# Kernel tuning notes

Hardware: AMD Instinct MI355X
Metric: run time of the kernel (lower is better)

The kernel has to match this reference:

```python
import jax, jax.numpy as jnp
import numpy as np

H = 56; W = 56; WS = 7; SHIFT = 3; C = 128; NH = 4; HD = C // NH
N = WS * WS; NW = (H // WS) * (W // WS); B = 64; HID = 4 * C
ALPHA = (1, 2, 4, 8); SCALE = HD ** -0.5


def _rel_index_np():
    coords = np.stack(np.meshgrid(np.arange(WS), np.arange(WS), indexing="ij"))
    cf = coords.reshape(2, -1)
    rel = (cf[:, :, None] - cf[:, None, :]).transpose(1, 2, 0).copy()
    rel[:, :, 0] += WS - 1
    rel[:, :, 1] += WS - 1
    rel[:, :, 0] *= 2 * WS - 1
    return rel.sum(-1).astype(np.int32)  # (N, N)


def _attn_mask_np():
    img = np.zeros((1, H, W, 1), np.float32)
    cnt = 0
    sl = (slice(0, -WS), slice(-WS, -SHIFT), slice(-SHIFT, None))
    for hs in sl:
        for ws in sl:
            img[:, hs, ws, :] = cnt
            cnt += 1
    mw = img.reshape(1, H // WS, WS, W // WS, WS, 1).transpose(0, 1, 3, 2, 4, 5).reshape(-1, N)
    am = mw[:, None, :] - mw[:, :, None]
    return np.where(am != 0, -100.0, 0.0).astype(np.float32)  # (NW, N, N)


def setup_inputs() -> dict:
    key = jax.random.key(0)
    ks = jax.random.split(key, 8)
    p = lambda k, shp, s=0.02: jax.random.normal(k, shp, jnp.float32) * s
    return {
        "x": jax.random.normal(ks[0], (B, H * W, C), jnp.float32),
        "gumbel_weights": jax.nn.softmax(jax.random.normal(ks[1], (4,), jnp.float32)),
        "norm1_w": jnp.ones((C,), jnp.float32), "norm1_b": jnp.zeros((C,), jnp.float32),
        "qkv_w": p(ks[2], (3 * C, C)), "qkv_b": jnp.zeros((3 * C,), jnp.float32),
        "rel_bias_table": p(ks[3], ((2 * WS - 1) ** 2, NH)),
        "proj_w": p(ks[4], (C, C)), "proj_b": jnp.zeros((C,), jnp.float32),
        "attn_mask": jnp.asarray(_attn_mask_np()),
        "norm2_w": jnp.ones((C,), jnp.float32), "norm2_b": jnp.zeros((C,), jnp.float32),
        "fc1_w": p(ks[5], (HID, C)), "fc1_b": jnp.zeros((HID,), jnp.float32),
        "fc2_w": p(ks[6], (C, HID)), "fc2_b": jnp.zeros((C,), jnp.float32),
        "rel_index": jnp.asarray(_rel_index_np()),
    }


def _ln(x, w, b, eps=1e-5):
    mu = x.mean(-1, keepdims=True)
    var = ((x - mu) ** 2).mean(-1, keepdims=True)
    return (x - mu) * jax.lax.rsqrt(var + eps) * w + b


def _win_part(x):  # (B,H,W,C) -> (B*NW, N, C)
    b = x.shape[0]
    x = x.reshape(b, H // WS, WS, W // WS, WS, C).transpose(0, 1, 3, 2, 4, 5)
    return x.reshape(-1, N, C)


def _win_rev(w, b):  # (b*NW, N, C) -> (b,H,W,C)
    x = w.reshape(b, H // WS, W // WS, WS, WS, C).transpose(0, 1, 3, 2, 4, 5)
    return x.reshape(b, H, W, C)


def _window_attn(xw, qkv_w, qkv_b, bias, mask, proj_w, proj_b):
    b = xw.shape[0]
    qkv = (xw @ qkv_w.T + qkv_b).reshape(b, N, 3, NH, HD).transpose(2, 0, 3, 1, 4)
    q, k, v = qkv[0] * SCALE, qkv[1], qkv[2]  # (b,NH,N,HD)
    a = jnp.einsum("bhnd,bhmd->bhnm", q, k) + bias[None]
    a = (a.reshape(b // NW, NW, NH, N, N) + mask[None, :, None]).reshape(b, NH, N, N)
    a = jax.nn.softmax(a, axis=-1)
    o = jnp.einsum("bhnm,bhmd->bhnd", a, v).transpose(0, 2, 1, 3).reshape(b, N, C)
    return o @ proj_w.T + proj_b


def _forward(x, gw, n1w, n1b, qkv_w, qkv_b, rbt, pw, pb, am, n2w, n2b, f1w, f1b, f2w, f2b, rel_index):
    shortcut = x
    xs = _ln(x, n1w, n1b).reshape(B, H, W, C)
    xs = jnp.roll(xs, (-SHIFT, -SHIFT), axis=(1, 2))  # cyclic shift
    xw = _win_part(xs)  # (B*NW, N, C)
    bias = rbt[rel_index.reshape(-1)].reshape(N, N, NH).transpose(2, 0, 1)  # (NH,N,N)
    half = xw.shape[0] // 2
    xw_l, xw_s = xw[:half], xw[half:]
    # large half: full-width window attention
    y_l = _window_attn(xw_l, qkv_w, qkv_b, bias, am, pw, pb)
    # small half: gumbel-gated slimmable branches (zero channels beyond C//alpha in/out)
    ch = jnp.arange(C)
    y_s = jnp.zeros_like(xw_s)
    for i, a in enumerate(ALPHA):
        if a > NH:
            continue
        cm = (ch < C // a).astype(xw.dtype)
        yb = _window_attn(xw_s * cm, qkv_w, qkv_b, bias, am, pw, pb) * cm
        y_s = y_s + yb * gw[i]
    attn_out = jnp.concatenate([y_l, y_s], axis=0)
    xr = _win_rev(attn_out, B)
    xr = jnp.roll(xr, (SHIFT, SHIFT), axis=(1, 2)).reshape(B, H * W, C)
    x = shortcut + xr
    # MLP with gumbel-gated slimmable small half (matches Mlp.forward)
    xn = _ln(x, n2w, n2b)
    xn_l, xn_s = xn[: B // 2], xn[B // 2 :]
    m_l = jax.nn.gelu(xn_l @ f1w.T + f1b, approximate=False) @ f2w.T + f2b
    m_s = jnp.zeros_like(xn_s)
    for i, a in enumerate(ALPHA):
        if a > NH:
            continue
        cm = (ch < C // a).astype(xn.dtype)
        yb = (jax.nn.gelu((xn_s * cm) @ f1w.T + f1b, approximate=False) @ f2w.T + f2b) * cm
        m_s = m_s + yb * gw[i]
    mlp_out = jnp.concatenate([m_l, m_s], axis=0)
    return x + mlp_out


def reference(x, gumbel_weights, norm1_w, norm1_b, qkv_w, qkv_b, rel_bias_table, proj_w, proj_b, attn_mask, norm2_w, norm2_b, fc1_w, fc1_b, fc2_w, fc2_b, rel_index):
    return _forward(x, gumbel_weights, norm1_w, norm1_b, qkv_w, qkv_b, rel_bias_table, proj_w, proj_b, attn_mask, norm2_w, norm2_b, fc1_w, fc1_b, fc2_w, fc2_b, rel_index)
```

## Files before the change

kernel.cpp:

```cpp
#include <hip/hip_runtime.h>
#include <hip/hip_bf16.h>

#define SHIFT_ 3
#define SCALE_ 0.17677669529663687f
#define NTOK   200704
#define NWIN   4096

typedef short v8s __attribute__((ext_vector_type(8)));
typedef float v4f __attribute__((ext_vector_type(4)));
#define MFMA16(a, b, c) __builtin_amdgcn_mfma_f32_16x16x32_bf16(a, b, c, 0, 0, 0)

static __device__ __forceinline__ unsigned short f2bf(float f) {
    union { float f; unsigned int u; } v; v.f = f;
    unsigned int u = v.u;
    unsigned int r = u + 0x7FFFu + ((u >> 16) & 1u);
    return (unsigned short)(r >> 16);
}
static __device__ __forceinline__ float wsum(float v) {
    #pragma unroll
    for (int o = 32; o; o >>= 1) v += __shfl_xor(v, o);
    return v;
}
static __device__ __forceinline__ float gelu_f(float v) {
    float w = v * v;
    float t = v * fmaf(w, 0.07135481283f, 1.595769122f);
    float e = __expf(-t);
    return v * __builtin_amdgcn_rcpf(1.f + e);
}

#define WS_COMB  67108864
#define WS_WQKV  71303168
#define WS_WPROJ 71401472
#define WS_F1W   71434240
#define WS_F2W   71565312

__global__ __launch_bounds__(256) void k_prep(
    const float* __restrict__ amask, const float* __restrict__ rbt,
    const int* __restrict__ relidx,
    const float* __restrict__ qkvw, const float* __restrict__ projw,
    const float* __restrict__ f1w, const float* __restrict__ f2w,
    float* __restrict__ comb, unsigned short* __restrict__ wqkv,
    unsigned short* __restrict__ wproj, unsigned short* __restrict__ f1wb,
    unsigned short* __restrict__ f2wb, unsigned short* __restrict__ xw) {
    int idx = blockIdx.x * 256 + threadIdx.x;
    if (idx < 1048576) {
        int wpos = idx >> 14;
        int h = (idx >> 12) & 3;
        int i = (idx >> 6) & 63;
        int j = idx & 63;
        float v;
        if (j >= 49) v = -1e30f;
        else if (i >= 49) v = 0.f;
        else v = amask[wpos * 2401 + i * 49 + j] + rbt[relidx[i * 49 + j] * 4 + h];
        comb[idx] = v;
    } else if (idx < 1048576 + 49152) {
        int k = idx - 1048576; wqkv[k] = f2bf(qkvw[k]);
    } else if (idx < 1048576 + 49152 + 16384) {
        int k = idx - (1048576 + 49152); wproj[k] = f2bf(projw[k]);
    } else if (idx < 1048576 + 49152 + 16384 + 65536) {
        int k = idx - (1048576 + 49152 + 16384); f1wb[k] = f2bf(f1w[k]);
    } else if (idx < 1048576 + 49152 + 16384 + 65536 + 65536) {
        int k = idx - (1048576 + 49152 + 16384 + 65536); f2wb[k] = f2bf(f2w[k]);
    } else {
        int k = idx - 1245184;
        if (k < 983040) {
            int win = k / 240, r = k - win * 240;
            uint4 z = make_uint4(0u, 0u, 0u, 0u);
            *(uint4*)((char*)xw + (size_t)win * 16384 + 12544 + (size_t)r * 16) = z;
        }
    }
}

__global__ __launch_bounds__(256) void k_ln1(const float* __restrict__ x,
                                             const float* __restrict__ nw,
                                             const float* __restrict__ nb,
                                             unsigned short* __restrict__ xw) {
    int tok  = blockIdx.x * 4 + (threadIdx.x >> 6);
    int lane = threadIdx.x & 63;
    int win = tok / 49, t = tok - win * 49;
    int bb = win >> 6, wh = (win >> 3) & 7, ww = win & 7;
    int i = t / 7, j = t - i * 7;
    int h  = wh * 7 + i + SHIFT_; if (h  >= 56) h  -= 56;
    int w2 = ww * 7 + j + SHIFT_; if (w2 >= 56) w2 -= 56;
    const float* src = x + ((size_t)bb * 3136 + h * 56 + w2) * 128;
    float v0 = src[lane], v1 = src[lane + 64];
    float mu = wsum(v0 + v1) * (1.f / 128.f);
    float d0 = v0 - mu, d1 = v1 - mu;
    float var = wsum(d0 * d0 + d1 * d1) * (1.f / 128.f);
    float inv = rsqrtf(var + 1e-5f);
    unsigned short* dst = xw + (size_t)win * 8192 + t * 128;
    dst[lane]      = f2bf(d0 * inv * nw[lane]      + nb[lane]);
    dst[lane + 64] = f2bf(d1 * inv * nw[lane + 64] + nb[lane + 64]);
}

__global__ __launch_bounds__(256) void k_ln2(const float* __restrict__ x2,
                                             const float* __restrict__ nw,
                                             const float* __restrict__ nb,
                                             unsigned short* __restrict__ xn) {
    int tok  = blockIdx.x * 4 + (threadIdx.x >> 6);
    int lane = threadIdx.x & 63;
    const float* src = x2 + (size_t)tok * 128;
    float v0 = src[lane], v1 = src[lane + 64];
    float mu = wsum(v0 + v1) * (1.f / 128.f);
    float d0 = v0 - mu, d1 = v1 - mu;
    float var = wsum(d0 * d0 + d1 * d1) * (1.f / 128.f);
    float inv = rsqrtf(var + 1e-5f);
    unsigned short* dst = xn + (size_t)tok * 128;
    dst[lane]      = f2bf(d0 * inv * nw[lane]      + nb[lane]);
    dst[lane + 64] = f2bf(d1 * inv * nw[lane + 64] + nb[lane + 64]);
}

template<int KA>
__device__ __forceinline__ void attn_pass(
    const v8s (&ax)[4][4],
    const unsigned short* __restrict__ wqkv, const float* __restrict__ qkvb,
    const float* __restrict__ comb,
    const unsigned short* __restrict__ wproj, const float* __restrict__ pbias,
    float wgt, int wpos, int wv, int li, int lg,
    unsigned short* __restrict__ s_q, unsigned short* __restrict__ s_k,
    unsigned short* __restrict__ s_v, unsigned short* __restrict__ pw_,
    v4f (&yacc)[2][4])
{
    const v4f z4 = {0.f, 0.f, 0.f, 0.f};
    constexpr int Ca = KA * 32;

    #pragma unroll 2
    for (int nt = 0; nt < 6; nt++) {
        const int ntg = wv * 6 + nt, o0 = ntg * 16;
        v4f acc[4] = {z4, z4, z4, z4};
        #pragma unroll
        for (int k = 0; k < KA; k++) {
            v8s b = *(const v8s*)(wqkv + (o0 + li) * 128 + k * 32 + lg * 8);
            #pragma unroll
            for (int m = 0; m < 4; m++) acc[m] = MFMA16(ax[m][k], b, acc[m]);
        }
        float bo = qkvb[o0 + li];
        if (ntg < 16) {
            unsigned short* dst = (ntg < 8) ? s_q : s_k;
            const int oc = (ntg < 8) ? o0 : o0 - 128;
            const float scl = (ntg < 8) ? SCALE_ : 1.f;
            #pragma unroll
            for (int m = 0; m < 4; m++)
                #pragma unroll
                for (int r = 0; r < 4; r++)
                    dst[(m * 16 + lg * 4 + r) * 136 + oc + li] =
                        f2bf((acc[m][r] + bo) * scl);
        } else {
            const int d = (ntg - 16) * 16 + li;
            #pragma unroll
            for (int m = 0; m < 4; m++) {
                int t0_ = m * 16 + lg * 4;
                unsigned int p0 = (unsigned int)f2bf(acc[m][0] + bo) |
                                  ((unsigned int)f2bf(acc[m][1] + bo) << 16);
                unsigned int p1 = (unsigned int)f2bf(acc[m][2] + bo) |
                                  ((unsigned int)f2bf(acc[m][3] + bo) << 16);
                *(unsigned int*)(s_v + d * 72 + t0_)     = p0;
                *(unsigned int*)(s_v + d * 72 + t0_ + 2) = p1;
            }
        }
    }
    __syncthreads();

    v4f oacc[8];
    #pragma unroll
    for (int i = 0; i < 8; i++) oacc[i] = z4;
    #pragma unroll
    for (int h = 0; h < 4; h++) {
        v8s aq = *(const v8s*)(s_q + (wv * 16 + li) * 136 + h * 32 + lg * 8);
        v4f sc[4];
        #pragma unroll
        for (int ntj = 0; ntj < 4; ntj++) {
            v8s bk = *(const v8s*)(s_k + (ntj * 16 + li) * 136 + h * 32 + lg * 8);
            sc[ntj] = MFMA16(aq, bk, z4);
        }
        const float* cb = comb + ((size_t)(wpos * 4 + h) << 12) + (wv * 16 + lg * 4) * 64;
        #pragma unroll
        for (int r = 0; r < 4; r++) {
            float vmax = -3.0e38f, e[4];
            #pragma unroll
            for (int ntj = 0; ntj < 4; ntj++) {
                float v_ = sc[ntj][r] + cb[r * 64 + ntj * 16 + li];
                sc[ntj][r] = v_;
                vmax = fmaxf(vmax, v_);
            }
            #pragma unroll
            for (int o_ = 1; o_ < 16; o_ <<= 1) vmax = fmaxf(vmax, __shfl_xor(vmax, o_));
            float ssum = 0.f;
            #pragma unroll
            for (int ntj = 0; ntj < 4; ntj++) {
                e[ntj] = __expf(sc[ntj][r] - vmax);
                ssum += e[ntj];
            }
            #pragma unroll
            for (int o_ = 1; o_ < 16; o_ <<= 1) ssum += __shfl_xor(ssum, o_);
            float inv = __builtin_amdgcn_rcpf(ssum);
            #pragma unroll
            for (int ntj = 0; ntj < 4; ntj++)
                pw_[(lg * 4 + r) * 72 + ntj * 16 + li] = f2bf(e[ntj] * inv);
        }
        #pragma unroll
        for (int k0 = 0; k0 < 2; k0++) {
            v8s ap = *(const v8s*)(pw_ + li * 72 + k0 * 32 + lg * 8);
            #pragma unroll
            for (int dn = 0; dn < 2; dn++) {
                v8s bv = *(const v8s*)(s_v + (h * 32 + dn * 16 + li) * 72 + k0 * 32 + lg * 8);
                oacc[h * 2 + dn] = MFMA16(ap, bv, oacc[h * 2 + dn]);
            }
        }
    }
    __syncthreads();

    unsigned short* s_o = s_k;
    #pragma unroll
    for (int ot = 0; ot < 8; ot++)
        #pragma unroll
        for (int r = 0; r < 4; r++)
            s_o[(wv * 16 + lg * 4 + r) * 136 + ot * 16 + li] = f2bf(oacc[ot][r]);
    __syncthreads();

    if (KA == 4 || wv * 16 < Ca) {
        v8s ao[4][4];
        #pragma unroll
        for (int m = 0; m < 4; m++)
            #pragma unroll
            for (int k = 0; k < 4; k++)
                ao[m][k] = *(const v8s*)(s_o + (m * 16 + li) * 136 + k * 32 + lg * 8);
        #pragma unroll
        for (int nt = 0; nt < 2; nt++) {
            const int co0 = (nt * 4 + wv) * 16;
            if (nt == 0 || Ca == 128) {
                if (co0 < Ca) {
                    v4f pacc[4] = {z4, z4, z4, z4};
                    #pragma unroll
                    for (int k = 0; k < 4; k++) {
                        v8s b = *(const v8s*)(wproj + (co0 + li) * 128 + k * 32 + lg * 8);
                        #pragma unroll
                        for (int m = 0; m < 4; m++) pacc[m] = MFMA16(ao[m][k], b, pacc[m]);
                    }
                    float bo = pbias[co0 + li];
                    #pragma unroll
                    for (int m = 0; m < 4; m++)
                        #pragma unroll
                        for (int r = 0; r < 4; r++)
                            yacc[nt][m][r] += wgt * (pacc[m][r] + bo);
                }
            }
        }
    }
    __syncthreads();
}

__global__ __launch_bounds__(256, 2) void k_attn(
    const unsigned short* __restrict__ xw,
    const unsigned short* __restrict__ wqkv, const float* __restrict__ qkvb,
    const float* __restrict__ comb,
    const unsigned short* __restrict__ wproj, const float* __restrict__ pbias,
    const float* __restrict__ gw,
    const float* __restrict__ x, float* __restrict__ out) {

    __shared__ unsigned short sm[31232];
    unsigned short* s_q = sm;
    unsigned short* s_k = sm + 8704;
    unsigned short* s_v = sm + 17408;
    unsigned short* s_p = sm + 26624;

    const int tid = threadIdx.x, wv = tid >> 6, lane = tid & 63;
    const int li = lane & 15, lg = lane >> 4;
    const int w = blockIdx.x;
    const int wpos = w & 63;
    const bool sp = (w >= 2048);
    const unsigned short* xwin = xw + (size_t)w * 8192;
    unsigned short* pw_ = s_p + wv * 1152;

    const v4f z4 = {0.f, 0.f, 0.f, 0.f};
    v4f yacc[2][4];
    #pragma unroll
    for (int n = 0; n < 2; n++)
        #pragma unroll
        for (int m = 0; m < 4; m++) yacc[n][m] = z4;

    v8s ax[4][4];
    #pragma unroll
    for (int m = 0; m < 4; m++)
        #pragma unroll
        for (int k = 0; k < 4; k++)
            ax[m][k] = *(const v8s*)(xwin + (m * 16 + li) * 128 + k * 32 + lg * 8);

    if (sp) {
        attn_pass<4>(ax, wqkv, qkvb, comb, wproj, pbias, gw[0], wpos, wv, li, lg,
                     s_q, s_k, s_v, pw_, yacc);
        attn_pass<2>(ax, wqkv, qkvb, comb, wproj, pbias, gw[1], wpos, wv, li, lg,
                     s_q, s_k, s_v, pw_, yacc);
        attn_pass<1>(ax, wqkv, qkvb, comb, wproj, pbias, gw[2], wpos, wv, li, lg,
                     s_q, s_k, s_v, pw_, yacc);
    } else {
        attn_pass<4>(ax, wqkv, qkvb, comb, wproj, pbias, 1.f, wpos, wv, li, lg,
                     s_q, s_k, s_v, pw_, yacc);
    }

    float* s_y = (float*)sm;
    #pragma unroll
    for (int m = 0; m < 4; m++)
        #pragma unroll
        for (int r = 0; r < 4; r++) {
            int t = m * 16 + lg * 4 + r;
            #pragma unroll
            for (int nt = 0; nt < 2; nt++)
                s_y[t * 132 + (nt * 4 + wv) * 16 + li] = yacc[nt][m][r];
        }
    __syncthreads();

    const int bb = w >> 6, wh = (w >> 3) & 7, ww = w & 7;
    const int rgrp = tid >> 5;
    const int col  = (tid & 31) * 4;
    #pragma unroll
    for (int it = 0; it < 7; it++) {
        int t = it * 8 + rgrp;
        if (t < 49) {
            int ti = t / 7, tj = t - ti * 7;
            int h2 = wh * 7 + ti + SHIFT_; if (h2 >= 56) h2 -= 56;
            int w2 = ww * 7 + tj + SHIFT_; if (w2 >= 56) w2 -= 56;
            size_t base = ((size_t)bb * 3136 + h2 * 56 + w2) * 128 + col;
            v4f xv = *(const v4f*)(x + base);
            v4f yv = *(const v4f*)(s_y + t * 132 + col);
            *(v4f*)(out + base) = xv + yv;
        }
    }
}

template<int KA>
__device__ __forceinline__ void mlp_pass(
    const v8s (&ax)[2][4],
    const unsigned short* __restrict__ f1wb, const float* __restrict__ f1b,
    const unsigned short* __restrict__ f2wb, const float* __restrict__ f2b,
    float wgt, int wv, int li, int lg,
    unsigned short* __restrict__ s_h, v4f (&yacc)[2][2])
{
    const v4f z4 = {0.f, 0.f, 0.f, 0.f};
    constexpr int Ca = KA * 32;

    #pragma unroll 4
    for (int nt = 0; nt < 8; nt++) {
        const int o0 = wv * 128 + nt * 16;
        v4f acc[2] = {z4, z4};
        #pragma unroll
        for (int k = 0; k < KA; k++) {
            v8s b = *(const v8s*)(f1wb + (o0 + li) * 128 + k * 32 + lg * 8);
            acc[0] = MFMA16(ax[0][k], b, acc[0]);
            acc[1] = MFMA16(ax[1][k], b, acc[1]);
        }
        float bo = f1b[o0 + li];
        const int chb = (o0 >> 3) + (li >> 3);
        const int clo = li & 7;
        #pragma unroll
        for (int m = 0; m < 2; m++)
            #pragma unroll
            for (int r = 0; r < 4; r++) {
                float g = gelu_f(acc[m][r] + bo);
                int row = m * 16 + lg * 4 + r;
                s_h[row * 512 + ((chb ^ (row & 7)) << 3) + clo] = f2bf(g);
            }
    }
    __syncthreads();

    if (KA == 4) {
        const int c0 = wv * 16, c1 = 64 + wv * 16;
        v4f acc2[2][2] = {{z4, z4}, {z4, z4}};
        #pragma unroll
        for (int k = 0; k < 16; k++) {
            const int sw = ((4 * k + lg) ^ (li & 7)) << 3;
            v8s a0 = *(const v8s*)(s_h + li * 512 + sw);
            v8s a1 = *(const v8s*)(s_h + (16 + li) * 512 + sw);
            v8s b0 = *(const v8s*)(f2wb + (c0 + li) * 512 + k * 32 + lg * 8);
            v8s b1 = *(const v8s*)(f2wb + (c1 + li) * 512 + k * 32 + lg * 8);
            acc2[0][0] = MFMA16(a0, b0, acc2[0][0]);
            acc2[0][1] = MFMA16(a1, b0, acc2[0][1]);
            acc2[1][0] = MFMA16(a0, b1, acc2[1][0]);
            acc2[1][1] = MFMA16(a1, b1, acc2[1][1]);
        }
        float bo0 = f2b[c0 + li], bo1 = f2b[c1 + li];
        #pragma unroll
        for (int m = 0; m < 2; m++)
            #pragma unroll
            for (int r = 0; r < 4; r++) {
                yacc[0][m][r] += wgt * (acc2[0][m][r] + bo0);
                yacc[1][m][r] += wgt * (acc2[1][m][r] + bo1);
            }
    } else if (KA == 2 || wv < 2) {
        const int c0 = wv * 16;
        v4f acc2[2] = {z4, z4};
        #pragma unroll
        for (int k = 0; k < 16; k++) {
            const int sw = ((4 * k + lg) ^ (li & 7)) << 3;
            v8s a0 = *(const v8s*)(s_h + li * 512 + sw);
            v8s a1 = *(const v8s*)(s_h + (16 + li) * 512 + sw);
            v8s b0 = *(const v8s*)(f2wb + (c0 + li) * 512 + k * 32 + lg * 8);
            acc2[0] = MFMA16(a0, b0, acc2[0]);
            acc2[1] = MFMA16(a1, b0, acc2[1]);
        }
        float bo0 = f2b[c0 + li];
        #pragma unroll
        for (int m = 0; m < 2; m++)
            #pragma unroll
            for (int r = 0; r < 4; r++)
                yacc[0][m][r] += wgt * (acc2[m][r] + bo0);
    }
}

__global__ __launch_bounds__(256, 5) void k_mlp(
    const unsigned short* __restrict__ xn,
    const unsigned short* __restrict__ f1wb, const float* __restrict__ f1b,
    const unsigned short* __restrict__ f2wb, const float* __restrict__ f2b,
    const float* __restrict__ gw, float* __restrict__ out) {

    __shared__ unsigned short s_h[32 * 512];

    const int tid = threadIdx.x, wv = tid >> 6, lane = tid & 63;
    const int li = lane & 15, lg = lane >> 4;
    const int t0 = blockIdx.x * 32;
    const bool sp = (t0 >= 100352);

    const v4f z4 = {0.f, 0.f, 0.f, 0.f};
    v4f yacc[2][2];
    #pragma unroll
    for (int n = 0; n < 2; n++)
        #pragma unroll
        for (int m = 0; m < 2; m++) yacc[n][m] = z4;

    v8s ax[2][4];
    #pragma unroll
    for (int m = 0; m < 2; m++)
        #pragma unroll
        for (int k = 0; k < 4; k++)
            ax[m][k] = *(const v8s*)(xn + (size_t)(t0 + m * 16 + li) * 128 + k * 32 + lg * 8);

    if (sp) {
        mlp_pass<4>(ax, f1wb, f1b, f2wb, f2b, gw[0], wv, li, lg, s_h, yacc);
        __syncthreads();
        mlp_pass<2>(ax, f1wb, f1b, f2wb, f2b, gw[1], wv, li, lg, s_h, yacc);
        __syncthreads();
        mlp_pass<1>(ax, f1wb, f1b, f2wb, f2b, gw[2], wv, li, lg, s_h, yacc);
    } else {
        mlp_pass<4>(ax, f1wb, f1b, f2wb, f2b, 1.f, wv, li, lg, s_h, yacc);
    }

    __syncthreads();
    float* s_y = (float*)s_h;
    #pragma unroll
    for (int m = 0; m < 2; m++)
        #pragma unroll
        for (int r = 0; r < 4; r++) {
            int t = m * 16 + lg * 4 + r;
            #pragma unroll
            for (int nt = 0; nt < 2; nt++)
                s_y[t * 132 + (nt * 4 + wv) * 16 + li] = yacc[nt][m][r];
        }
    __syncthreads();

    const int rgrp = tid >> 5;
    const int col  = (tid & 31) * 4;
    #pragma unroll
    for (int it = 0; it < 4; it++) {
        int t = it * 8 + rgrp;
        size_t base = (size_t)(t0 + t) * 128 + col;
        v4f ov = *(const v4f*)(out + base);
        v4f yv = *(const v4f*)(s_y + t * 132 + col);
        *(v4f*)(out + base) = ov + yv;
    }
}

extern "C" void kernel_launch(void* const* d_in, const int* in_sizes, int n_in,
                              void* d_out, int out_size, void* d_ws, size_t ws_size,
                              hipStream_t stream) {
    const float* x      = (const float*)d_in[0];
    const float* gw     = (const float*)d_in[1];
    const float* n1w    = (const float*)d_in[2];
    const float* n1b    = (const float*)d_in[3];
    const float* qkvw   = (const float*)d_in[4];
    const float* qkvb   = (const float*)d_in[5];
    const float* rbt    = (const float*)d_in[6];
    const float* pw     = (const float*)d_in[7];
    const float* pb     = (const float*)d_in[8];
    const float* amask  = (const float*)d_in[9];
    const float* n2w    = (const float*)d_in[10];
    const float* n2b    = (const float*)d_in[11];
    const float* f1w    = (const float*)d_in[12];
    const float* f1b    = (const float*)d_in[13];
    const float* f2w    = (const float*)d_in[14];
    const float* f2b    = (const float*)d_in[15];
    const int*   relidx = (const int*)d_in[16];
    float* out = (float*)d_out;

    unsigned short* xw    = (unsigned short*)d_ws;
    float*          comb  = (float*)((char*)d_ws + WS_COMB);
    unsigned short* wqkv  = (unsigned short*)((char*)d_ws + WS_WQKV);
    unsigned short* wproj = (unsigned short*)((char*)d_ws + WS_WPROJ);
    unsigned short* f1wb  = (unsigned short*)((char*)d_ws + WS_F1W);
    unsigned short* f2wb  = (unsigned short*)((char*)d_ws + WS_F2W);
    unsigned short* xn    = (unsigned short*)d_ws;

    hipLaunchKernelGGL(k_prep, dim3(8704), dim3(256), 0, stream,
                       amask, rbt, relidx, qkvw, pw, f1w, f2w,
                       comb, wqkv, wproj, f1wb, f2wb, xw);
    hipLaunchKernelGGL(k_ln1, dim3(NTOK / 4), dim3(256), 0, stream, x, n1w, n1b, xw);
    hipLaunchKernelGGL(k_attn, dim3(NWIN), dim3(256), 0, stream,
                       xw, wqkv, qkvb, comb, wproj, pb, gw, x, out);
    hipLaunchKernelGGL(k_ln2, dim3(NTOK / 4), dim3(256), 0, stream, out, n2w, n2b, xn);
    hipLaunchKernelGGL(k_mlp, dim3(NTOK / 32), dim3(256), 0, stream,
                       xn, f1wb, f1b, f2wb, f2b, gw, out);
}
```

Before: 799.9 us.

## Retile MLP kernel to 64 tokens per block with 8 waves

The MLP kernel now processes 64 tokens per block using 512 threads (8 waves) instead of 32 tokens with 4 waves. Each wave now computes a 64-wide hidden slice for all four 16-row token groups in fc1 and one 16-column output slice in fc2. This doubles weight reuse per fetched B fragment and reduces total weight traffic from L2. In exchange LDS per block doubles to 64 KB and the register pressure per wave changes, which can reduce occupancy. The input activations are now reloaded from global memory for each gumbel pass.

Result: slower. 998.0 us (+24.8%).

```diff
diff --git a/kernel.cpp b/kernel.cpp
--- a/kernel.cpp
+++ b/kernel.cpp
@@ -330,138 +330,110 @@
 
 template<int KA>
 __device__ __forceinline__ void mlp_pass(
-    const v8s (&ax)[2][4],
+    const unsigned short* __restrict__ xn, int t0,
     const unsigned short* __restrict__ f1wb, const float* __restrict__ f1b,
     const unsigned short* __restrict__ f2wb, const float* __restrict__ f2b,
     float wgt, int wv, int li, int lg,
-    unsigned short* __restrict__ s_h, v4f (&yacc)[2][2])
+    unsigned short* __restrict__ s_h, v4f (&yacc)[4])
 {
     const v4f z4 = {0.f, 0.f, 0.f, 0.f};
     constexpr int Ca = KA * 32;
 
-    #pragma unroll 4
-    for (int nt = 0; nt < 8; nt++) {
-        const int o0 = wv * 128 + nt * 16;
-        v4f acc[2] = {z4, z4};
-        #pragma unroll
-        for (int k = 0; k < KA; k++) {
-            v8s b = *(const v8s*)(f1wb + (o0 + li) * 128 + k * 32 + lg * 8);
-            acc[0] = MFMA16(ax[0][k], b, acc[0]);
-            acc[1] = MFMA16(ax[1][k], b, acc[1]);
-        }
-        float bo = f1b[o0 + li];
-        const int chb = (o0 >> 3) + (li >> 3);
-        const int clo = li & 7;
-        #pragma unroll
-        for (int m = 0; m < 2; m++)
-            #pragma unroll
-            for (int r = 0; r < 4; r++) {
-                float g = gelu_f(acc[m][r] + bo);
-                int row = m * 16 + lg * 4 + r;
-                s_h[row * 512 + ((chb ^ (row & 7)) << 3) + clo] = f2bf(g);
-            }
-    }
-    __syncthreads();
-
-    if (KA == 4) {
-        const int c0 = wv * 16, c1 = 64 + wv * 16;
-        v4f acc2[2][2] = {{z4, z4}, {z4, z4}};
+    {
+        v8s ax[4][KA];
+        #pragma unroll
+        for (int m = 0; m < 4; m++)
+            #pragma unroll
+            for (int k = 0; k < KA; k++)
+                ax[m][k] = *(const v8s*)(xn + (size_t)(t0 + m * 16 + li) * 128 + k * 32 + lg * 8);
+
+        #pragma unroll
+        for (int nt = 0; nt < 4; nt++) {
+            const int o0 = wv * 64 + nt * 16;
+            v4f acc[4] = {z4, z4, z4, z4};
+            #pragma unroll
+            for (int k = 0; k < KA; k++) {
+                v8s b = *(const v8s*)(f1wb + (o0 + li) * 128 + k * 32 + lg * 8);
+                #pragma unroll
+                for (int m = 0; m < 4; m++) acc[m] = MFMA16(ax[m][k], b, acc[m]);
+            }
+            float bo = f1b[o0 + li];
+            const int chb = (o0 >> 3) + (li >> 3);
+            const int clo = li & 7;
+            #pragma unroll
+            for (int m = 0; m < 4; m++)
+                #pragma unroll
+                for (int r = 0; r < 4; r++) {
+                    float g = gelu_f(acc[m][r] + bo);
+                    int row = m * 16 + lg * 4 + r;
+                    s_h[row * 512 + ((chb ^ (row & 7)) << 3) + clo] = f2bf(g);
+                }
+        }
+    }
+    __syncthreads();
+
+    if (KA == 4 || wv * 16 < Ca) {
+        const int c0 = wv * 16;
+        v4f acc2[4] = {z4, z4, z4, z4};
         #pragma unroll
         for (int k = 0; k < 16; k++) {
             const int sw = ((4 * k + lg) ^ (li & 7)) << 3;
-            v8s a0 = *(const v8s*)(s_h + li * 512 + sw);
-            v8s a1 = *(const v8s*)(s_h + (16 + li) * 512 + sw);
             v8s b0 = *(const v8s*)(f2wb + (c0 + li) * 512 + k * 32 + lg * 8);
-            v8s b1 = *(const v8s*)(f2wb + (c1 + li) * 512 + k * 32 + lg * 8);
-            acc2[0][0] = MFMA16(a0, b0, acc2[0][0]);
-            acc2[0][1] = MFMA16(a1, b0, acc2[0][1]);
-            acc2[1][0] = MFMA16(a0, b1, acc2[1][0]);
-            acc2[1][1] = MFMA16(a1, b1, acc2[1][1]);
-        }
-        float bo0 = f2b[c0 + li], bo1 = f2b[c1 + li];
-        #pragma unroll
-        for (int m = 0; m < 2; m++)
-            #pragma unroll
-            for (int r = 0; r < 4; r++) {
-                yacc[0][m][r] += wgt * (acc2[0][m][r] + bo0);
-                yacc[1][m][r] += wgt * (acc2[1][m][r] + bo1);
-            }
-    } else if (KA == 2 || wv < 2) {
-        const int c0 = wv * 16;
-        v4f acc2[2] = {z4, z4};
-        #pragma unroll
-        for (int k = 0; k < 16; k++) {
-            const int sw = ((4 * k + lg) ^ (li & 7)) << 3;
-            v8s a0 = *(const v8s*)(s_h + li * 512 + sw);
-            v8s a1 = *(const v8s*)(s_h + (16 + li) * 512 + sw);
-            v8s b0 = *(const v8s*)(f2wb + (c0 + li) * 512 + k * 32 + lg * 8);
-            acc2[0] = MFMA16(a0, b0, acc2[0]);
-            acc2[1] = MFMA16(a1, b0, acc2[1]);
-        }
-        float bo0 = f2b[c0 + li];
-        #pragma unroll
-        for (int m = 0; m < 2; m++)
+            #pragma unroll
+            for (int m = 0; m < 4; m++) {
+                v8s a = *(const v8s*)(s_h + (m * 16 + li) * 512 + sw);
+                acc2[m] = MFMA16(a, b0, acc2[m]);
+            }
+        }
+        float bo = f2b[c0 + li];
+        #pragma unroll
+        for (int m = 0; m < 4; m++)
             #pragma unroll
             for (int r = 0; r < 4; r++)
-                yacc[0][m][r] += wgt * (acc2[m][r] + bo0);
-    }
-}
-
-__global__ __launch_bounds__(256, 5) void k_mlp(
+                yacc[m][r] += wgt * (acc2[m][r] + bo);
+    }
+}
+
+__global__ __launch_bounds__(512, 4) void k_mlp(
     const unsigned short* __restrict__ xn,
     const unsigned short* __restrict__ f1wb, const float* __restrict__ f1b,
     const unsigned short* __restrict__ f2wb, const float* __restrict__ f2b,
     const float* __restrict__ gw, float* __restrict__ out) {
 
-    __shared__ unsigned short s_h[32 * 512];
+    __shared__ unsigned short s_h[64 * 512];
 
     const int tid = threadIdx.x, wv = tid >> 6, lane = tid & 63;
     const int li = lane & 15, lg = lane >> 4;
-    const int t0 = blockIdx.x * 32;
+    const int t0 = blockIdx.x * 64;
     const bool sp = (t0 >= 100352);
 
     const v4f z4 = {0.f, 0.f, 0.f, 0.f};
-    v4f yacc[2][2];
-    #pragma unroll
-    for (int n = 0; n < 2; n++)
-        #pragma unroll
-        for (int m = 0; m < 2; m++) yacc[n][m] = z4;
-
-    v8s ax[2][4];
-    #pragma unroll
-    for (int m = 0; m < 2; m++)
-        #pragma unroll
-        for (int k = 0; k < 4; k++)
-            ax[m][k] = *(const v8s*)(xn + (size_t)(t0 + m * 16 + li) * 128 + k * 32 + lg * 8);
+    v4f yacc[4] = {z4, z4, z4, z4};
 
     if (sp) {
-        mlp_pass<4>(ax, f1wb, f1b, f2wb, f2b, gw[0], wv, li, lg, s_h, yacc);
+        mlp_pass<4>(xn, t0, f1wb, f1b, f2wb, f2b, gw[0], wv, li, lg, s_h, yacc);
         __syncthreads();
-        mlp_pass<2>(ax, f1wb, f1b, f2wb, f2b, gw[1], wv, li, lg, s_h, yacc);
+        mlp_pass<2>(xn, t0, f1wb, f1b, f2wb, f2b, gw[1], wv, li, lg, s_h, yacc);
         __syncthreads();
-        mlp_pass<1>(ax, f1wb, f1b, f2wb, f2b, gw[2], wv, li, lg, s_h, yacc);
+        mlp_pass<1>(xn, t0, f1wb, f1b, f2wb, f2b, gw[2], wv, li, lg, s_h, yacc);
     } else {
-        mlp_pass<4>(ax, f1wb, f1b, f2wb, f2b, 1.f, wv, li, lg, s_h, yacc);
+        mlp_pass<4>(xn, t0, f1wb, f1b, f2wb, f2b, 1.f, wv, li, lg, s_h, yacc);
     }
 
     __syncthreads();
     float* s_y = (float*)s_h;
     #pragma unroll
-    for (int m = 0; m < 2; m++)
-        #pragma unroll
-        for (int r = 0; r < 4; r++) {
-            int t = m * 16 + lg * 4 + r;
-            #pragma unroll
-            for (int nt = 0; nt < 2; nt++)
-                s_y[t * 132 + (nt * 4 + wv) * 16 + li] = yacc[nt][m][r];
-        }
+    for (int m = 0; m < 4; m++)
+        #pragma unroll
+        for (int r = 0; r < 4; r++)
+            s_y[(m * 16 + lg * 4 + r) * 132 + wv * 16 + li] = yacc[m][r];
     __syncthreads();
 
     const int rgrp = tid >> 5;
     const int col  = (tid & 31) * 4;
     #pragma unroll
     for (int it = 0; it < 4; it++) {
-        int t = it * 8 + rgrp;
+        int t = it * 16 + rgrp;
         size_t base = (size_t)(t0 + t) * 128 + col;
         v4f ov = *(const v4f*)(out + base);
         v4f yv = *(const v4f*)(s_y + t * 132 + col);
@@ -506,6 +478,6 @@
     hipLaunchKernelGGL(k_attn, dim3(NWIN), dim3(256), 0, stream,
                        xw, wqkv, qkvb, comb, wproj, pb, gw, x, out);
     hipLaunchKernelGGL(k_ln2, dim3(NTOK / 4), dim3(256), 0, stream, out, n2w, n2b, xn);
-    hipLaunchKernelGGL(k_mlp, dim3(NTOK / 32), dim3(256), 0, stream,
+    hipLaunchKernelGGL(k_mlp, dim3(NTOK / 64), dim3(512), 0, stream,
                        xn, f1wb, f1b, f2wb, f2b, gw, out);
 }
```
